# Kernel optimization log

Hardware: AMD Instinct MI355X
Metric: run time of the kernel (lower is better)

## Reference

```python
import jax, jax.numpy as jnp
import numpy as np

STRIDE = 1
PAD = 1
DIL = 1


def setup_inputs() -> dict:
    key = jax.random.key(0)
    k1, k2, k3, k4 = jax.random.split(key, 4)
    N, Cin, H, W = 4, 256, 64, 64
    Cout, kh, kw = 256, 3, 3
    inputs = jax.random.normal(k1, (N, Cin, H, W), jnp.float32)
    filter = jax.random.normal(k2, (Cout, Cin, kh, kw), jnp.float32) * 0.05
    # offsets in pixels (y,x interleaved per tap), typical magnitude O(1)
    offset = jax.random.normal(k3, (N, 2 * kh * kw, H, W), jnp.float32)
    # modulation mask in [0,1) (post-sigmoid in real nets)
    mask = jax.random.uniform(k4, (N, kh * kw, H, W), jnp.float32)
    return {"inputs": inputs, "filter": filter, "offset": offset, "mask": mask}


def _dcn_forward(inputs, filt, offset, mask):
    N, C, H, W = inputs.shape
    Cout, _, kh, kw = filt.shape
    K = kh * kw
    Ho = (H + 2 * PAD - DIL * (kh - 1) - 1) // STRIDE + 1
    Wo = (W + 2 * PAD - DIL * (kw - 1) - 1) // STRIDE + 1

    # base sampling grid per kernel tap: [K, Ho, Wo]
    ki, kj = jnp.meshgrid(jnp.arange(kh), jnp.arange(kw), indexing='ij')
    ki = ki.reshape(K, 1, 1)
    kj = kj.reshape(K, 1, 1)
    base_y = (jnp.arange(Ho)[None, :, None] * STRIDE - PAD + ki * DIL).astype(jnp.float32)
    base_x = (jnp.arange(Wo)[None, None, :] * STRIDE - PAD + kj * DIL).astype(jnp.float32)

    # offset channels: per tap k, channel 2k = dy, channel 2k+1 = dx
    off = offset.reshape(N, K, 2, Ho, Wo)
    y = base_y[None] + off[:, :, 0]  # [N, K, Ho, Wo]
    x = base_x[None] + off[:, :, 1]

    y0 = jnp.floor(y)
    x0 = jnp.floor(x)
    ly = y - y0  # fractional parts, [N, K, Ho, Wo]
    lx = x - x0
    y0i = y0.astype(jnp.int32)
    x0i = x0.astype(jnp.int32)

    def gather(img, yy, xx):
        # img [C,H,W]; yy,xx [K,Ho,Wo] int; zero outside bounds
        valid = (yy >= 0) & (yy < H) & (xx >= 0) & (xx < W)
        yc = jnp.clip(yy, 0, H - 1)
        xc = jnp.clip(xx, 0, W - 1)
        return img[:, yc, xc] * valid.astype(img.dtype)  # [C,K,Ho,Wo]

    def sample_one(img, y0i, x0i, ly, lx):
        v00 = gather(img, y0i, x0i)
        v01 = gather(img, y0i, x0i + 1)
        v10 = gather(img, y0i + 1, x0i)
        v11 = gather(img, y0i + 1, x0i + 1)
        return (v00 * (1 - ly) * (1 - lx) + v01 * (1 - ly) * lx
                + v10 * ly * (1 - lx) + v11 * ly * lx)

    # bilinear-sampled, modulated im2col columns: [N, C, K, Ho, Wo]
    col = jax.vmap(sample_one)(inputs, y0i, x0i, ly, lx)
    col = col * mask.reshape(N, 1, K, Ho, Wo)

    # grouped conv with num_groups=1: plain GEMM over (C, K)
    out = jnp.einsum('ock,nckhw->nohw', filt.reshape(Cout, C, K), col)
    return out


def reference(inputs, filter, offset, mask):
    return _dcn_forward(inputs, filter, offset, mask)
```

## Files before the change

kernel.cpp:

```cpp
#include <hip/hip_runtime.h>
#include <stdint.h>

typedef __attribute__((ext_vector_type(2))) float f32x2;
typedef __attribute__((ext_vector_type(4))) float f32x4;
typedef __attribute__((ext_vector_type(8))) short bf16x8;

static constexpr int N_ = 4, C_ = 256, HW_ = 4096;
static constexpr int CO_ = 256, KTAP = 9, KK = 2304;
static constexpr int NSTEP = 72;
static constexpr int A_STEP_BYTES = 16 * 64 * 16;

static constexpr size_t NHWC_BYTES = (size_t)N_ * HW_ * C_ * 2;
static constexpr size_t ABF_OFF    = NHWC_BYTES;
static constexpr size_t ABF_BYTES  = (size_t)NSTEP * A_STEP_BYTES;

__device__ inline unsigned f2bf(float f) {
  unsigned u = __builtin_bit_cast(unsigned, f);
  unsigned r = u + 0x7FFFu + ((u >> 16) & 1u);
  return r >> 16;
}
__device__ inline float asf(unsigned u) { return __builtin_bit_cast(float, u); }

__global__ __launch_bounds__(256) void k_nchw_to_nhwc(const float* __restrict__ in,
                                                      unsigned short* __restrict__ nhwc) {
  __shared__ float tile[64][65];
  int b = blockIdx.x;
  int n = b >> 8, cg = (b >> 6) & 3, hwg = b & 63;
  int c0 = cg * 64, hw0 = hwg * 64;
  int t = threadIdx.x;
  int col = t & 63, r0 = t >> 6;
#pragma unroll
  for (int i = 0; i < 16; ++i) {
    int row = r0 + i * 4;
    tile[row][col] = in[(size_t)(n * C_ + c0 + row) * HW_ + hw0 + col];
  }
  __syncthreads();
  int pr = t >> 2, cc0 = (t & 3) * 16;
  unsigned us[8];
#pragma unroll
  for (int i = 0; i < 8; ++i) {
    unsigned lo = f2bf(tile[cc0 + 2 * i][pr]);
    unsigned hi = f2bf(tile[cc0 + 2 * i + 1][pr]);
    us[i] = lo | (hi << 16);
  }
  unsigned* dst = (unsigned*)(nhwc + (size_t)(n * HW_ + hw0 + pr) * C_ + c0 + cc0);
  ((uint4*)dst)[0] = make_uint4(us[0], us[1], us[2], us[3]);
  ((uint4*)dst)[1] = make_uint4(us[4], us[5], us[6], us[7]);
}

__global__ __launch_bounds__(256) void k_prep_filter(const float* __restrict__ filt,
                                                     unsigned short* __restrict__ abf2) {
  int gid = blockIdx.x * 256 + threadIdx.x;
  int o = gid >> 8, c = gid & 255;
  const float* f = filt + (size_t)(o * C_ + c) * KTAP;
  int rb = o >> 4;
  int lane = ((c >> 3) & 3) * 16 + (o & 15);
  int j = c & 7;
#pragma unroll
  for (int tap = 0; tap < KTAP; ++tap) {
    int s = tap * 8 + (c >> 5);
    abf2[((size_t)(s * 16 + rb) * 64 + lane) * 8 + j] = (unsigned short)f2bf(f[tap]);
  }
}

struct GB { uint4 g[4]; f32x4 w; };

__device__ __forceinline__ f32x2 unpk(unsigned u) {
  return (f32x2){asf(u << 16), asf(u & 0xffff0000u)};
}

__device__ __forceinline__ void buildB8(const GB& b, char* dst) {
  f32x2 r0 = b.w.x * unpk(b.g[0].x) + b.w.y * unpk(b.g[1].x) +
             b.w.z * unpk(b.g[2].x) + b.w.w * unpk(b.g[3].x);
  f32x2 r1 = b.w.x * unpk(b.g[0].y) + b.w.y * unpk(b.g[1].y) +
             b.w.z * unpk(b.g[2].y) + b.w.w * unpk(b.g[3].y);
  f32x2 r2 = b.w.x * unpk(b.g[0].z) + b.w.y * unpk(b.g[1].z) +
             b.w.z * unpk(b.g[2].z) + b.w.w * unpk(b.g[3].z);
  f32x2 r3 = b.w.x * unpk(b.g[0].w) + b.w.y * unpk(b.g[1].w) +
             b.w.z * unpk(b.g[2].w) + b.w.w * unpk(b.g[3].w);
  unsigned o0, o1, o2, o3;
  asm("v_cvt_pk_bf16_f32 %0, %1, %2" : "=v"(o0) : "v"(r0.x), "v"(r0.y));
  asm("v_cvt_pk_bf16_f32 %0, %1, %2" : "=v"(o1) : "v"(r1.x), "v"(r1.y));
  asm("v_cvt_pk_bf16_f32 %0, %1, %2" : "=v"(o2) : "v"(r2.x), "v"(r2.y));
  asm("v_cvt_pk_bf16_f32 %0, %1, %2" : "=v"(o3) : "v"(r3.x), "v"(r3.y));
  *(uint4*)dst = make_uint4(o0, o1, o2, o3);
}

#define MFMA_BF16 __builtin_amdgcn_mfma_f32_16x16x32_bf16

#define PIPE(S, RDP, WRP, GCON, GISS, AC0, AC1, AN0, AN1)                      \
  do {                                                                         \
    if (cons) {                                                                \
      int s1_ = (S) + 1 < NSTEP ? (S) + 1 : NSTEP - 1;                         \
      AN0 = *(const bf16x8*)(aoff0 + (size_t)s1_ * A_STEP_BYTES);              \
      AN1 = *(const bf16x8*)(aoff1 + (size_t)s1_ * A_STEP_BYTES);              \
      const char* bb_ = (const char*)&Bl[0][0] + (RDP) * 4096;                 \
      bf16x8 b0_ = *(const bf16x8*)(bb_ + bo0);                                \
      bf16x8 b1_ = *(const bf16x8*)(bb_ + bo1);                                \
      __builtin_amdgcn_s_setprio(1);                                           \
      acc[0][0] = MFMA_BF16(AC0, b0_, acc[0][0], 0, 0, 0);                     \
      acc[1][0] = MFMA_BF16(AC1, b0_, acc[1][0], 0, 0, 0);                     \
      acc[0][1] = MFMA_BF16(AC0, b1_, acc[0][1], 0, 0, 0);                     \
      acc[1][1] = MFMA_BF16(AC1, b1_, acc[1][1], 0, 0, 0);                     \
      __builtin_amdgcn_s_setprio(0);                                           \
      bf16x8 b2_ = *(const bf16x8*)(bb_ + bo2);                                \
      bf16x8 b3_ = *(const bf16x8*)(bb_ + bo3);                                \
      __builtin_amdgcn_s_setprio(1);                                           \
      acc[0][2] = MFMA_BF16(AC0, b2_, acc[0][2], 0, 0, 0);                     \
      acc[1][2] = MFMA_BF16(AC1, b2_, acc[1][2], 0, 0, 0);                     \
      acc[0][3] = MFMA_BF16(AC0, b3_, acc[0][3], 0, 0, 0);                     \
      acc[1][3] = MFMA_BF16(AC1, b3_, acc[1][3], 0, 0, 0);                     \
      __builtin_amdgcn_s_setprio(0);                                           \
    } else {                                                                   \
      int s2_ = (S) + 2 < NSTEP ? (S) + 2 : NSTEP - 1;                         \
      if ((s2_ & 7) == 0) {                                                    \
        int tp_ = s2_ >> 3;                                                    \
        uint4 ra_ = *(const uint4*)&recA[(tp_ * 64 + p_b) * 4];                \
        wS = *(const f32x4*)&recW[(tp_ * 64 + p_b) * 4];                       \
        vS.x = ra_.x + kq16; vS.y = ra_.y + kq16;                              \
        vS.z = ra_.z + kq16; vS.w = ra_.w + kq16;                              \
      }                                                                        \
      unsigned co_ = (unsigned)((s2_ & 7) * 64);                               \
      GISS.g[0] = *(const uint4*)(nb_u + vS.x + co_);                          \
      GISS.g[1] = *(const uint4*)(nb_u + vS.y + co_);                          \
      GISS.g[2] = *(const uint4*)(nb_u + vS.z + co_);                          \
      GISS.g[3] = *(const uint4*)(nb_u + vS.w + co_);                          \
      GISS.w = wS;                                                             \
      buildB8(GCON, bwp + (WRP) * 4096);                                       \
      asm volatile("s_waitcnt lgkmcnt(0)" ::: "memory");                       \
    }                                                                          \
    asm volatile("" ::: "memory");                                             \
    __builtin_amdgcn_s_barrier();                                              \
    asm volatile("" ::: "memory");                                             \
  } while (0)

__global__ __launch_bounds__(768, 3) void k_dcn_gemm(const unsigned short* __restrict__ nhwc,
                                                     const unsigned short* __restrict__ abf2,
                                                     const float* __restrict__ offs,
                                                     const float* __restrict__ msk,
                                                     float* __restrict__ out) {
  __shared__ __align__(16) unsigned short Bl[2][2048];
  __shared__ float recW[KTAP * 64 * 4];
  __shared__ unsigned recA[KTAP * 64 * 4];

  int bid = blockIdx.x;
  int b = ((bid & 7) << 5) | (bid >> 3);
  int n = b >> 6;
  int ho = b & 63;
  int hw0 = ho << 6;
  int t = threadIdx.x;

  for (int r = t; r < 576; r += 768) {
    int pl = r / 9;
    int tap = r - pl * 9;
    int hw = hw0 + pl;
    float dy = offs[(size_t)(n * 18 + 2 * tap) * HW_ + hw];
    float dx = offs[(size_t)(n * 18 + 2 * tap + 1) * HW_ + hw];
    float mk = msk[(size_t)(n * 9 + tap) * HW_ + hw];
    float y = (float)(ho - 1 + tap / 3) + dy;
    float x = (float)(pl - 1 + tap % 3) + dx;
    float fy = floorf(y), fx = floorf(x);
    float ly = y - fy, lx = x - fx;
    int y0 = (int)fy, x0 = (int)fx;
    int y1 = y0 + 1, x1 = x0 + 1;
    float vy0 = (y0 >= 0 && y0 < 64) ? 1.f : 0.f;
    float vy1 = (y1 >= 0 && y1 < 64) ? 1.f : 0.f;
    float vx0 = (x0 >= 0 && x0 < 64) ? 1.f : 0.f;
    float vx1 = (x1 >= 0 && x1 < 64) ? 1.f : 0.f;
    int y0c = min(max(y0, 0), 63), y1c = min(max(y1, 0), 63);
    int x0c = min(max(x0, 0), 63), x1c = min(max(x1, 0), 63);
    int base = (tap * 64 + pl) * 4;
    recW[base + 0] = (1.f - ly) * (1.f - lx) * mk * vy0 * vx0;
    recW[base + 1] = (1.f - ly) * lx * mk * vy0 * vx1;
    recW[base + 2] = ly * (1.f - lx) * mk * vy1 * vx0;
    recW[base + 3] = ly * lx * mk * vy1 * vx1;
    recA[base + 0] = (unsigned)((y0c * 64 + x0c) * 512);
    recA[base + 1] = (unsigned)((y0c * 64 + x1c) * 512);
    recA[base + 2] = (unsigned)((y1c * 64 + x0c) * 512);
    recA[base + 3] = (unsigned)((y1c * 64 + x1c) * 512);
  }
  __syncthreads();

  int lane = t & 63, wv = t >> 6;
  bool cons = wv < 8;

  const char* aoff0 = (const char*)abf2 + ((wv * 2 + 0) * 64 + lane) * 16;
  const char* aoff1 = aoff0 + 1024;
  int cqr = lane >> 4;
  int pxl = lane & 15;
  const int bo0 = cqr * 1024 + ((((0 * 16 + pxl) + cqr * 5) & 63) * 16);
  const int bo1 = cqr * 1024 + ((((1 * 16 + pxl) + cqr * 5) & 63) * 16);
  const int bo2 = cqr * 1024 + ((((2 * 16 + pxl) + cqr * 5) & 63) * 16);
  const int bo3 = cqr * 1024 + ((((3 * 16 + pxl) + cqr * 5) & 63) * 16);

  int p_b = (t >> 2) & 63;
  int kq = t & 3;
  unsigned kq16 = (unsigned)(kq * 16);
  const char* nb_u = (const char*)nhwc + (size_t)n * HW_ * C_ * 2;
  char* bwp = (char*)&Bl[0][0] + (kq * 1024 + ((p_b + kq * 5) & 63) * 16);

  f32x4 acc[2][4];
#pragma unroll
  for (int mi = 0; mi < 2; ++mi)
#pragma unroll
    for (int ni = 0; ni < 4; ++ni) acc[mi][ni] = (f32x4){0.f, 0.f, 0.f, 0.f};

  GB gA, gB;
  bf16x8 afc0, afc1, afn0, afn1;
  uint4 vS;
  f32x4 wS;

  if (cons) {
    afc0 = *(const bf16x8*)(aoff0);
    afc1 = *(const bf16x8*)(aoff1);
  } else {
    uint4 ra0 = *(const uint4*)&recA[p_b * 4];
    wS = *(const f32x4*)&recW[p_b * 4];
    vS.x = ra0.x + kq16; vS.y = ra0.y + kq16;
    vS.z = ra0.z + kq16; vS.w = ra0.w + kq16;
    gA.g[0] = *(const uint4*)(nb_u + vS.x);
    gA.g[1] = *(const uint4*)(nb_u + vS.y);
    gA.g[2] = *(const uint4*)(nb_u + vS.z);
    gA.g[3] = *(const uint4*)(nb_u + vS.w);
    gA.w = wS;
    gB.g[0] = *(const uint4*)(nb_u + vS.x + 64);
    gB.g[1] = *(const uint4*)(nb_u + vS.y + 64);
    gB.g[2] = *(const uint4*)(nb_u + vS.z + 64);
    gB.g[3] = *(const uint4*)(nb_u + vS.w + 64);
    gB.w = wS;
    buildB8(gA, bwp);
    asm volatile("s_waitcnt lgkmcnt(0)" ::: "memory");
  }
  asm volatile("" ::: "memory");
  __builtin_amdgcn_s_barrier();
  asm volatile("" ::: "memory");

  for (int s = 0; s < NSTEP; s += 2) {
    PIPE(s,     0, 1, gB, gA, afc0, afc1, afn0, afn1);
    PIPE(s + 1, 1, 0, gA, gB, afn0, afn1, afc0, afc1);
  }

  if (cons) {
    float* ob = out + (size_t)n * CO_ * HW_ + hw0;
#pragma unroll
    for (int mi = 0; mi < 2; ++mi)
#pragma unroll
      for (int ni = 0; ni < 4; ++ni)
#pragma unroll
        for (int jj = 0; jj < 4; ++jj) {
          int o = wv * 32 + mi * 16 + (lane >> 4) * 4 + jj;
          int hw = ni * 16 + (lane & 15);
          ob[(size_t)o * HW_ + hw] = acc[mi][ni][jj];
        }
  }
}

extern "C" void kernel_launch(void* const* d_in, const int* in_sizes, int n_in,
                              void* d_out, int out_size, void* d_ws, size_t ws_size,
                              hipStream_t stream) {
  const float* inp  = (const float*)d_in[0];
  const float* filt = (const float*)d_in[1];
  const float* offs = (const float*)d_in[2];
  const float* msk  = (const float*)d_in[3];
  float* out = (float*)d_out;
  if (ws_size < ABF_OFF + ABF_BYTES) return;
  unsigned short* nhwc = (unsigned short*)d_ws;
  unsigned short* abf2 = (unsigned short*)((char*)d_ws + ABF_OFF);

  k_nchw_to_nhwc<<<1024, 256, 0, stream>>>(inp, nhwc);
  k_prep_filter<<<256, 256, 0, stream>>>(filt, abf2);
  k_dcn_gemm<<<256, 768, 0, stream>>>(nhwc, abf2, offs, msk, out);
}
```

Measured before the change: 53.93 us.

## Double pipeline step depth to K=64 and merge prep kernels into one launch

The GEMM main loop now handles two 32-wide K planes per step, so there are 36 steps instead of 72. The LDS B buffer doubles, producer waves issue eight 16-byte gathers per step, and consumers run sixteen MFMAs per barrier. The aim is to halve the number of barriers and pipeline handoffs. The two preprocessing kernels are also fused into one launch to save a kernel launch. In exchange, register pressure goes up in both producer and consumer waves, which may hurt occupancy at 768 threads with 3 blocks per CU.

```diff
diff --git a/kernel.cpp b/kernel.cpp
--- a/kernel.cpp
+++ b/kernel.cpp
@@ -7,12 +7,12 @@
 
 static constexpr int N_ = 4, C_ = 256, HW_ = 4096;
 static constexpr int CO_ = 256, KTAP = 9, KK = 2304;
-static constexpr int NSTEP = 72;
-static constexpr int A_STEP_BYTES = 16 * 64 * 16;
+static constexpr int NST = 36;
+static constexpr int A_PLANE = 16 * 64 * 16;
 
 static constexpr size_t NHWC_BYTES = (size_t)N_ * HW_ * C_ * 2;
 static constexpr size_t ABF_OFF    = NHWC_BYTES;
-static constexpr size_t ABF_BYTES  = (size_t)NSTEP * A_STEP_BYTES;
+static constexpr size_t ABF_BYTES  = (size_t)72 * A_PLANE;
 
 __device__ inline unsigned f2bf(float f) {
   unsigned u = __builtin_bit_cast(unsigned, f);
@@ -21,63 +21,63 @@
 }
 __device__ inline float asf(unsigned u) { return __builtin_bit_cast(float, u); }
 
-__global__ __launch_bounds__(256) void k_nchw_to_nhwc(const float* __restrict__ in,
-                                                      unsigned short* __restrict__ nhwc) {
-  __shared__ float tile[64][65];
+__global__ __launch_bounds__(256) void k_prep(const float* __restrict__ in,
+                                              const float* __restrict__ filt,
+                                              unsigned short* __restrict__ nhwc,
+                                              unsigned short* __restrict__ abf2) {
   int b = blockIdx.x;
-  int n = b >> 8, cg = (b >> 6) & 3, hwg = b & 63;
-  int c0 = cg * 64, hw0 = hwg * 64;
   int t = threadIdx.x;
-  int col = t & 63, r0 = t >> 6;
-#pragma unroll
-  for (int i = 0; i < 16; ++i) {
-    int row = r0 + i * 4;
-    tile[row][col] = in[(size_t)(n * C_ + c0 + row) * HW_ + hw0 + col];
-  }
-  __syncthreads();
-  int pr = t >> 2, cc0 = (t & 3) * 16;
-  unsigned us[8];
-#pragma unroll
-  for (int i = 0; i < 8; ++i) {
-    unsigned lo = f2bf(tile[cc0 + 2 * i][pr]);
-    unsigned hi = f2bf(tile[cc0 + 2 * i + 1][pr]);
-    us[i] = lo | (hi << 16);
-  }
-  unsigned* dst = (unsigned*)(nhwc + (size_t)(n * HW_ + hw0 + pr) * C_ + c0 + cc0);
-  ((uint4*)dst)[0] = make_uint4(us[0], us[1], us[2], us[3]);
-  ((uint4*)dst)[1] = make_uint4(us[4], us[5], us[6], us[7]);
-}
-
-__global__ __launch_bounds__(256) void k_prep_filter(const float* __restrict__ filt,
-                                                     unsigned short* __restrict__ abf2) {
-  int gid = blockIdx.x * 256 + threadIdx.x;
-  int o = gid >> 8, c = gid & 255;
-  const float* f = filt + (size_t)(o * C_ + c) * KTAP;
-  int rb = o >> 4;
-  int lane = ((c >> 3) & 3) * 16 + (o & 15);
-  int j = c & 7;
-#pragma unroll
-  for (int tap = 0; tap < KTAP; ++tap) {
-    int s = tap * 8 + (c >> 5);
-    abf2[((size_t)(s * 16 + rb) * 64 + lane) * 8 + j] = (unsigned short)f2bf(f[tap]);
-  }
-}
-
-struct GB { uint4 g[4]; f32x4 w; };
+  if (b < 1024) {
+    __shared__ float tile[64][65];
+    int n = b >> 8, cg = (b >> 6) & 3, hwg = b & 63;
+    int c0 = cg * 64, hw0 = hwg * 64;
+    int col = t & 63, r0 = t >> 6;
+#pragma unroll
+    for (int i = 0; i < 16; ++i) {
+      int row = r0 + i * 4;
+      tile[row][col] = in[(size_t)(n * C_ + c0 + row) * HW_ + hw0 + col];
+    }
+    __syncthreads();
+    int pr = t >> 2, cc0 = (t & 3) * 16;
+    unsigned us[8];
+#pragma unroll
+    for (int i = 0; i < 8; ++i) {
+      unsigned lo = f2bf(tile[cc0 + 2 * i][pr]);
+      unsigned hi = f2bf(tile[cc0 + 2 * i + 1][pr]);
+      us[i] = lo | (hi << 16);
+    }
+    unsigned* dst = (unsigned*)(nhwc + (size_t)(n * HW_ + hw0 + pr) * C_ + c0 + cc0);
+    ((uint4*)dst)[0] = make_uint4(us[0], us[1], us[2], us[3]);
+    ((uint4*)dst)[1] = make_uint4(us[4], us[5], us[6], us[7]);
+  } else {
+    int gid = (b - 1024) * 256 + t;
+    int o = gid >> 8, c = gid & 255;
+    const float* f = filt + (size_t)(o * C_ + c) * KTAP;
+    int rb = o >> 4;
+    int lane = ((c >> 3) & 3) * 16 + (o & 15);
+    int j = c & 7;
+#pragma unroll
+    for (int tap = 0; tap < KTAP; ++tap) {
+      int s32 = tap * 8 + (c >> 5);
+      abf2[((size_t)(s32 * 16 + rb) * 64 + lane) * 8 + j] = (unsigned short)f2bf(f[tap]);
+    }
+  }
+}
+
+struct GB2 { uint4 g[8]; f32x4 w; };
+struct AF  { bf16x8 f[4]; };
 
 __device__ __forceinline__ f32x2 unpk(unsigned u) {
   return (f32x2){asf(u << 16), asf(u & 0xffff0000u)};
 }
 
-__device__ __forceinline__ void buildB8(const GB& b, char* dst) {
-  f32x2 r0 = b.w.x * unpk(b.g[0].x) + b.w.y * unpk(b.g[1].x) +
-             b.w.z * unpk(b.g[2].x) + b.w.w * unpk(b.g[3].x);
-  f32x2 r1 = b.w.x * unpk(b.g[0].y) + b.w.y * unpk(b.g[1].y) +
-             b.w.z * unpk(b.g[2].y) + b.w.w * unpk(b.g[3].y);
-  f32x2 r2 = b.w.x * unpk(b.g[0].z) + b.w.y * unpk(b.g[1].z) +
-             b.w.z * unpk(b.g[2].z) + b.w.w * unpk(b.g[3].z);
-  f32x2 r3 = b.w.x * unpk(b.g[0].w) + b.w.y * unpk(b.g[1].w) +
-             b.w.z * unpk(b.g[2].w) + b.w.w * unpk(b.g[3].w);
+__device__ __forceinline__ void buildB8p(const uint4& g0, const uint4& g1,
+                                         const uint4& g2, const uint4& g3,
+                                         f32x4 w, char* dst) {
+  f32x2 r0 = w.x * unpk(g0.x) + w.y * unpk(g1.x) + w.z * unpk(g2.x) + w.w * unpk(g3.x);
+  f32x2 r1 = w.x * unpk(g0.y) + w.y * unpk(g1.y) + w.z * unpk(g2.y) + w.w * unpk(g3.y);
+  f32x2 r2 = w.x * unpk(g0.z) + w.y * unpk(g1.z) + w.z * unpk(g2.z) + w.w * unpk(g3.z);
+  f32x2 r3 = w.x * unpk(g0.w) + w.y * unpk(g1.w) + w.z * unpk(g2.w) + w.w * unpk(g3.w);
   unsigned o0, o1, o2, o3;
   asm("v_cvt_pk_bf16_f32 %0, %1, %2" : "=v"(o0) : "v"(r0.x), "v"(r0.y));
   asm("v_cvt_pk_bf16_f32 %0, %1, %2" : "=v"(o1) : "v"(r1.x), "v"(r1.y));
@@ -88,45 +88,68 @@
 
 #define MFMA_BF16 __builtin_amdgcn_mfma_f32_16x16x32_bf16
 
-#define PIPE(S, RDP, WRP, GCON, GISS, AC0, AC1, AN0, AN1)                      \
+#define PIPE(S, RDP, WRP, GCON, GISS, AC, AN)                                  \
   do {                                                                         \
     if (cons) {                                                                \
-      int s1_ = (S) + 1 < NSTEP ? (S) + 1 : NSTEP - 1;                         \
-      AN0 = *(const bf16x8*)(aoff0 + (size_t)s1_ * A_STEP_BYTES);              \
-      AN1 = *(const bf16x8*)(aoff1 + (size_t)s1_ * A_STEP_BYTES);              \
-      const char* bb_ = (const char*)&Bl[0][0] + (RDP) * 4096;                 \
-      bf16x8 b0_ = *(const bf16x8*)(bb_ + bo0);                                \
-      bf16x8 b1_ = *(const bf16x8*)(bb_ + bo1);                                \
+      int s1_ = (S) + 1 < NST ? (S) + 1 : NST - 1;                             \
+      const char* ab_ = aoff0 + (size_t)(2 * s1_) * A_PLANE;                   \
+      AN.f[0] = *(const bf16x8*)(ab_);                                         \
+      AN.f[1] = *(const bf16x8*)(ab_ + A_PLANE);                               \
+      AN.f[2] = *(const bf16x8*)(ab_ + 1024);                                  \
+      AN.f[3] = *(const bf16x8*)(ab_ + 1024 + A_PLANE);                        \
+      const char* bb_ = (const char*)&Bl[0][0] + (RDP) * 8192;                 \
+      bf16x8 b0_ = *(const bf16x8*)(bb_ + bo[0][0]);                           \
+      bf16x8 b1_ = *(const bf16x8*)(bb_ + bo[1][0]);                           \
+      bf16x8 b2_ = *(const bf16x8*)(bb_ + bo[2][0]);                           \
+      bf16x8 b3_ = *(const bf16x8*)(bb_ + bo[3][0]);                           \
       __builtin_amdgcn_s_setprio(1);                                           \
-      acc[0][0] = MFMA_BF16(AC0, b0_, acc[0][0], 0, 0, 0);                     \
-      acc[1][0] = MFMA_BF16(AC1, b0_, acc[1][0], 0, 0, 0);                     \
-      acc[0][1] = MFMA_BF16(AC0, b1_, acc[0][1], 0, 0, 0);                     \
-      acc[1][1] = MFMA_BF16(AC1, b1_, acc[1][1], 0, 0, 0);                     \
+      acc[0][0] = MFMA_BF16(AC.f[0], b0_, acc[0][0], 0, 0, 0);                 \
+      acc[1][0] = MFMA_BF16(AC.f[2], b0_, acc[1][0], 0, 0, 0);                 \
+      acc[0][1] = MFMA_BF16(AC.f[0], b1_, acc[0][1], 0, 0, 0);                 \
+      acc[1][1] = MFMA_BF16(AC.f[2], b1_, acc[1][1], 0, 0, 0);                 \
+      acc[0][2] = MFMA_BF16(AC.f[0], b2_, acc[0][2], 0, 0, 0);                 \
+      acc[1][2] = MFMA_BF16(AC.f[2], b2_, acc[1][2], 0, 0, 0);                 \
+      acc[0][3] = MFMA_BF16(AC.f[0], b3_, acc[0][3], 0, 0, 0);                 \
+      acc[1][3] = MFMA_BF16(AC.f[2], b3_, acc[1][3], 0, 0, 0);                 \
       __builtin_amdgcn_s_setprio(0);                                           \
-      bf16x8 b2_ = *(const bf16x8*)(bb_ + bo2);                                \
-      bf16x8 b3_ = *(const bf16x8*)(bb_ + bo3);                                \
+      bf16x8 b4_ = *(const bf16x8*)(bb_ + bo[0][1]);                           \
+      bf16x8 b5_ = *(const bf16x8*)(bb_ + bo[1][1]);                           \
+      bf16x8 b6_ = *(const bf16x8*)(bb_ + bo[2][1]);                           \
+      bf16x8 b7_ = *(const bf16x8*)(bb_ + bo[3][1]);                           \
       __builtin_amdgcn_s_setprio(1);                                           \
-      acc[0][2] = MFMA_BF16(AC0, b2_, acc[0][2], 0, 0, 0);                     \
-      acc[1][2] = MFMA_BF16(AC1, b2_, acc[1][2], 0, 0, 0);                     \
-      acc[0][3] = MFMA_BF16(AC0, b3_, acc[0][3], 0, 0, 0);                     \
-      acc[1][3] = MFMA_BF16(AC1, b3_, acc[1][3], 0, 0, 0);                     \
+      acc[0][0] = MFMA_BF16(AC.f[1], b4_, acc[0][0], 0, 0, 0);                 \
+      acc[1][0] = MFMA_BF16(AC.f[3], b4_, acc[1][0], 0, 0, 0);                 \
+      acc[0][1] = MFMA_BF16(AC.f[1], b5_, acc[0][1], 0, 0, 0);                 \
+      acc[1][1] = MFMA_BF16(AC.f[3], b5_, acc[1][1], 0, 0, 0);                 \
+      acc[0][2] = MFMA_BF16(AC.f[1], b6_, acc[0][2], 0, 0, 0);                 \
+      acc[1][2] = MFMA_BF16(AC.f[3], b6_, acc[1][2], 0, 0, 0);                 \
+      acc[0][3] = MFMA_BF16(AC.f[1], b7_, acc[0][3], 0, 0, 0);                 \
+      acc[1][3] = MFMA_BF16(AC.f[3], b7_, acc[1][3], 0, 0, 0);                 \
       __builtin_amdgcn_s_setprio(0);                                           \
     } else {                                                                   \
-      int s2_ = (S) + 2 < NSTEP ? (S) + 2 : NSTEP - 1;                         \
-      if ((s2_ & 7) == 0) {                                                    \
-        int tp_ = s2_ >> 3;                                                    \
+      int s2_ = (S) + 2 < NST ? (S) + 2 : NST - 1;                             \
+      if ((s2_ & 3) == 0) {                                                    \
+        int tp_ = s2_ >> 2;                                                    \
         uint4 ra_ = *(const uint4*)&recA[(tp_ * 64 + p_b) * 4];                \
         wS = *(const f32x4*)&recW[(tp_ * 64 + p_b) * 4];                       \
-        vS.x = ra_.x + kq16; vS.y = ra_.y + kq16;                              \
-        vS.z = ra_.z + kq16; vS.w = ra_.w + kq16;                              \
+        vS.x = ra_.x + kq32; vS.y = ra_.y + kq32;                              \
+        vS.z = ra_.z + kq32; vS.w = ra_.w + kq32;                              \
       }                                                                        \
-      unsigned co_ = (unsigned)((s2_ & 7) * 64);                               \
+      unsigned co_ = (unsigned)((s2_ & 3) * 128);                              \
       GISS.g[0] = *(const uint4*)(nb_u + vS.x + co_);                          \
-      GISS.g[1] = *(const uint4*)(nb_u + vS.y + co_);                          \
-      GISS.g[2] = *(const uint4*)(nb_u + vS.z + co_);                          \
-      GISS.g[3] = *(const uint4*)(nb_u + vS.w + co_);                          \
+      GISS.g[1] = *(const uint4*)(nb_u + vS.x + co_ + 16);                     \
+      GISS.g[2] = *(const uint4*)(nb_u + vS.y + co_);                          \
+      GISS.g[3] = *(const uint4*)(nb_u + vS.y + co_ + 16);                     \
+      GISS.g[4] = *(const uint4*)(nb_u + vS.z + co_);                          \
+      GISS.g[5] = *(const uint4*)(nb_u + vS.z + co_ + 16);                     \
+      GISS.g[6] = *(const uint4*)(nb_u + vS.w + co_);                          \
+      GISS.g[7] = *(const uint4*)(nb_u + vS.w + co_ + 16);                     \
       GISS.w = wS;                                                             \
-      buildB8(GCON, bwp + (WRP) * 4096);                                       \
+      __builtin_amdgcn_sched_barrier(0);                                       \
+      buildB8p(GCON.g[0], GCON.g[2], GCON.g[4], GCON.g[6], GCON.w,             \
+               bwp0 + (WRP) * 8192);                                           \
+      buildB8p(GCON.g[1], GCON.g[3], GCON.g[5], GCON.g[7], GCON.w,             \
+               bwp1 + (WRP) * 8192);                                           \
       asm volatile("s_waitcnt lgkmcnt(0)" ::: "memory");                       \
     }                                                                          \
     asm volatile("" ::: "memory");                                             \
@@ -139,7 +162,7 @@
                                                      const float* __restrict__ offs,
                                                      const float* __restrict__ msk,
                                                      float* __restrict__ out) {
-  __shared__ __align__(16) unsigned short Bl[2][2048];
+  __shared__ __align__(16) unsigned short Bl[2][4096];
   __shared__ float recW[KTAP * 64 * 4];
   __shared__ unsigned recA[KTAP * 64 * 4];
 
@@ -184,20 +207,26 @@
   int lane = t & 63, wv = t >> 6;
   bool cons = wv < 8;
 
-  const char* aoff0 = (const char*)abf2 + ((wv * 2 + 0) * 64 + lane) * 16;
-  const char* aoff1 = aoff0 + 1024;
-  int cqr = lane >> 4;
+  const char* aoff0 = (const char*)abf2 + ((wv * 2) * 64 + lane) * 16;
+  int q_r = lane >> 4;
   int pxl = lane & 15;
-  const int bo0 = cqr * 1024 + ((((0 * 16 + pxl) + cqr * 5) & 63) * 16);
-  const int bo1 = cqr * 1024 + ((((1 * 16 + pxl) + cqr * 5) & 63) * 16);
-  const int bo2 = cqr * 1024 + ((((2 * 16 + pxl) + cqr * 5) & 63) * 16);
-  const int bo3 = cqr * 1024 + ((((3 * 16 + pxl) + cqr * 5) & 63) * 16);
-
-  int p_b = (t >> 2) & 63;
-  int kq = t & 3;
-  unsigned kq16 = (unsigned)(kq * 16);
+  int bo[4][2];
+#pragma unroll
+  for (int ni = 0; ni < 4; ++ni)
+#pragma unroll
+    for (int h = 0; h < 2; ++h) {
+      int p = h * 4 + q_r;
+      bo[ni][h] = p * 1024 + (((pxl + 16 * ni) + 5 * p) & 63) * 16;
+    }
+
+  int pid = t - 512;
+  int p_b = (pid >> 2) & 63;
+  int kq = pid & 3;
+  unsigned kq32 = (unsigned)(kq * 32);
   const char* nb_u = (const char*)nhwc + (size_t)n * HW_ * C_ * 2;
-  char* bwp = (char*)&Bl[0][0] + (kq * 1024 + ((p_b + kq * 5) & 63) * 16);
+  int pl0 = 2 * kq, pl1 = 2 * kq + 1;
+  char* bwp0 = (char*)&Bl[0][0] + pl0 * 1024 + ((p_b + 5 * pl0) & 63) * 16;
+  char* bwp1 = (char*)&Bl[0][0] + pl1 * 1024 + ((p_b + 5 * pl1) & 63) * 16;
 
   f32x4 acc[2][4];
 #pragma unroll
@@ -205,39 +234,50 @@
 #pragma unroll
     for (int ni = 0; ni < 4; ++ni) acc[mi][ni] = (f32x4){0.f, 0.f, 0.f, 0.f};
 
-  GB gA, gB;
-  bf16x8 afc0, afc1, afn0, afn1;
+  GB2 gA, gB;
+  AF aC, aN;
   uint4 vS;
   f32x4 wS;
 
   if (cons) {
-    afc0 = *(const bf16x8*)(aoff0);
-    afc1 = *(const bf16x8*)(aoff1);
+    aC.f[0] = *(const bf16x8*)(aoff0);
+    aC.f[1] = *(const bf16x8*)(aoff0 + A_PLANE);
+    aC.f[2] = *(const bf16x8*)(aoff0 + 1024);
+    aC.f[3] = *(const bf16x8*)(aoff0 + 1024 + A_PLANE);
   } else {
     uint4 ra0 = *(const uint4*)&recA[p_b * 4];
     wS = *(const f32x4*)&recW[p_b * 4];
-    vS.x = ra0.x + kq16; vS.y = ra0.y + kq16;
-    vS.z = ra0.z + kq16; vS.w = ra0.w + kq16;
+    vS.x = ra0.x + kq32; vS.y = ra0.y + kq32;
+    vS.z = ra0.z + kq32; vS.w = ra0.w + kq32;
     gA.g[0] = *(const uint4*)(nb_u + vS.x);
-    gA.g[1] = *(const uint4*)(nb_u + vS.y);
-    gA.g[2] = *(const uint4*)(nb_u + vS.z);
-    gA.g[3] = *(const uint4*)(nb_u + vS.w);
+    gA.g[1] = *(const uint4*)(nb_u + vS.x + 16);
+    gA.g[2] = *(const uint4*)(nb_u + vS.y);
+    gA.g[3] = *(const uint4*)(nb_u + vS.y + 16);
+    gA.g[4] = *(const uint4*)(nb_u + vS.z);
+    gA.g[5] = *(const uint4*)(nb_u + vS.z + 16);
+    gA.g[6] = *(const uint4*)(nb_u + vS.w);
+    gA.g[7] = *(const uint4*)(nb_u + vS.w + 16);
     gA.w = wS;
-    gB.g[0] = *(const uint4*)(nb_u + vS.x + 64);
-    gB.g[1] = *(const uint4*)(nb_u + vS.y + 64);
-    gB.g[2] = *(const uint4*)(nb_u + vS.z + 64);
-    gB.g[3] = *(const uint4*)(nb_u + vS.w + 64);
+    gB.g[0] = *(const uint4*)(nb_u + vS.x + 128);
+    gB.g[1] = *(const uint4*)(nb_u + vS.x + 144);
+    gB.g[2] = *(const uint4*)(nb_u + vS.y + 128);
+    gB.g[3] = *(const uint4*)(nb_u + vS.y + 144);
+    gB.g[4] = *(const uint4*)(nb_u + vS.z + 128);
+    gB.g[5] = *(const uint4*)(nb_u + vS.z + 144);
+    gB.g[6] = *(const uint4*)(nb_u + vS.w + 128);
+    gB.g[7] = *(const uint4*)(nb_u + vS.w + 144);
     gB.w = wS;
-    buildB8(gA, bwp);
+    buildB8p(gA.g[0], gA.g[2], gA.g[4], gA.g[6], gA.w, bwp0);
+    buildB8p(gA.g[1], gA.g[3], gA.g[5], gA.g[7], gA.w, bwp1);
     asm volatile("s_waitcnt lgkmcnt(0)" ::: "memory");
   }
   asm volatile("" ::: "memory");
   __builtin_amdgcn_s_barrier();
   asm volatile("" ::: "memory");
 
-  for (int s = 0; s < NSTEP; s += 2) {
-    PIPE(s,     0, 1, gB, gA, afc0, afc1, afn0, afn1);
-    PIPE(s + 1, 1, 0, gA, gB, afn0, afn1, afc0, afc1);
+  for (int s = 0; s < NST; s += 2) {
+    PIPE(s,     0, 1, gB, gA, aC, aN);
+    PIPE(s + 1, 1, 0, gA, gB, aN, aC);
   }
 
   if (cons) {
@@ -267,7 +307,6 @@
   unsigned short* nhwc = (unsigned short*)d_ws;
   unsigned short* abf2 = (unsigned short*)((char*)d_ws + ABF_OFF);
 
-  k_nchw_to_nhwc<<<1024, 256, 0, stream>>>(inp, nhwc);
-  k_prep_filter<<<256, 256, 0, stream>>>(filt, abf2);
+  k_prep<<<1280, 256, 0, stream>>>(inp, filt, nhwc, abf2);
   k_dcn_gemm<<<256, 768, 0, stream>>>(nhwc, abf2, offs, msk, out);
 }
```

Result: slower. 74.65 us (+38.4%).

## Halve GEMM pixel tile to 32 for more blocks and merge prep kernels

Applied to the files above, without the earlier changes.

Each GEMM block now covers 32 output pixels (half a row) instead of 64, so the grid doubles to 512 blocks with 640 threads: 8 MFMA consumer waves and 2 gather/producer waves. LDS buffers, swizzles and accumulators shrink to match, and the launch bounds move to allow more resident blocks per CU. This targets poor occupancy and wave balance across the 256 CUs. The input layout transform and filter prep kernels are also fused into one launch to cut launch overhead. In exchange, A-fragment reuse per block is halved, so filter traffic doubles, and there is half as much gather work to hide latency behind.

```diff
diff --git a/kernel.cpp b/kernel.cpp
--- a/kernel.cpp
+++ b/kernel.cpp
@@ -8,11 +8,11 @@
 static constexpr int N_ = 4, C_ = 256, HW_ = 4096;
 static constexpr int CO_ = 256, KTAP = 9, KK = 2304;
 static constexpr int NSTEP = 72;
-static constexpr int A_STEP_BYTES = 16 * 64 * 16;
+static constexpr int A_PLANE = 16 * 64 * 16;
 
 static constexpr size_t NHWC_BYTES = (size_t)N_ * HW_ * C_ * 2;
 static constexpr size_t ABF_OFF    = NHWC_BYTES;
-static constexpr size_t ABF_BYTES  = (size_t)NSTEP * A_STEP_BYTES;
+static constexpr size_t ABF_BYTES  = (size_t)NSTEP * A_PLANE;
 
 __device__ inline unsigned f2bf(float f) {
   unsigned u = __builtin_bit_cast(unsigned, f);
@@ -21,45 +21,46 @@
 }
 __device__ inline float asf(unsigned u) { return __builtin_bit_cast(float, u); }
 
-__global__ __launch_bounds__(256) void k_nchw_to_nhwc(const float* __restrict__ in,
-                                                      unsigned short* __restrict__ nhwc) {
-  __shared__ float tile[64][65];
+__global__ __launch_bounds__(256) void k_prep(const float* __restrict__ in,
+                                              const float* __restrict__ filt,
+                                              unsigned short* __restrict__ nhwc,
+                                              unsigned short* __restrict__ abf2) {
   int b = blockIdx.x;
-  int n = b >> 8, cg = (b >> 6) & 3, hwg = b & 63;
-  int c0 = cg * 64, hw0 = hwg * 64;
   int t = threadIdx.x;
-  int col = t & 63, r0 = t >> 6;
-#pragma unroll
-  for (int i = 0; i < 16; ++i) {
-    int row = r0 + i * 4;
-    tile[row][col] = in[(size_t)(n * C_ + c0 + row) * HW_ + hw0 + col];
-  }
-  __syncthreads();
-  int pr = t >> 2, cc0 = (t & 3) * 16;
-  unsigned us[8];
-#pragma unroll
-  for (int i = 0; i < 8; ++i) {
-    unsigned lo = f2bf(tile[cc0 + 2 * i][pr]);
-    unsigned hi = f2bf(tile[cc0 + 2 * i + 1][pr]);
-    us[i] = lo | (hi << 16);
-  }
-  unsigned* dst = (unsigned*)(nhwc + (size_t)(n * HW_ + hw0 + pr) * C_ + c0 + cc0);
-  ((uint4*)dst)[0] = make_uint4(us[0], us[1], us[2], us[3]);
-  ((uint4*)dst)[1] = make_uint4(us[4], us[5], us[6], us[7]);
-}
-
-__global__ __launch_bounds__(256) void k_prep_filter(const float* __restrict__ filt,
-                                                     unsigned short* __restrict__ abf2) {
-  int gid = blockIdx.x * 256 + threadIdx.x;
-  int o = gid >> 8, c = gid & 255;
-  const float* f = filt + (size_t)(o * C_ + c) * KTAP;
-  int rb = o >> 4;
-  int lane = ((c >> 3) & 3) * 16 + (o & 15);
-  int j = c & 7;
-#pragma unroll
-  for (int tap = 0; tap < KTAP; ++tap) {
-    int s = tap * 8 + (c >> 5);
-    abf2[((size_t)(s * 16 + rb) * 64 + lane) * 8 + j] = (unsigned short)f2bf(f[tap]);
+  if (b < 1024) {
+    __shared__ float tile[64][65];
+    int n = b >> 8, cg = (b >> 6) & 3, hwg = b & 63;
+    int c0 = cg * 64, hw0 = hwg * 64;
+    int col = t & 63, r0 = t >> 6;
+#pragma unroll
+    for (int i = 0; i < 16; ++i) {
+      int row = r0 + i * 4;
+      tile[row][col] = in[(size_t)(n * C_ + c0 + row) * HW_ + hw0 + col];
+    }
+    __syncthreads();
+    int pr = t >> 2, cc0 = (t & 3) * 16;
+    unsigned us[8];
+#pragma unroll
+    for (int i = 0; i < 8; ++i) {
+      unsigned lo = f2bf(tile[cc0 + 2 * i][pr]);
+      unsigned hi = f2bf(tile[cc0 + 2 * i + 1][pr]);
+      us[i] = lo | (hi << 16);
+    }
+    unsigned* dst = (unsigned*)(nhwc + (size_t)(n * HW_ + hw0 + pr) * C_ + c0 + cc0);
+    ((uint4*)dst)[0] = make_uint4(us[0], us[1], us[2], us[3]);
+    ((uint4*)dst)[1] = make_uint4(us[4], us[5], us[6], us[7]);
+  } else {
+    int gid = (b - 1024) * 256 + t;
+    int o = gid >> 8, c = gid & 255;
+    const float* f = filt + (size_t)(o * C_ + c) * KTAP;
+    int rb = o >> 4;
+    int lane = ((c >> 3) & 3) * 16 + (o & 15);
+    int j = c & 7;
+#pragma unroll
+    for (int tap = 0; tap < KTAP; ++tap) {
+      int s = tap * 8 + (c >> 5);
+      abf2[((size_t)(s * 16 + rb) * 64 + lane) * 8 + j] = (unsigned short)f2bf(f[tap]);
+    }
   }
 }
 
@@ -92,9 +93,9 @@
   do {                                                                         \
     if (cons) {                                                                \
       int s1_ = (S) + 1 < NSTEP ? (S) + 1 : NSTEP - 1;                         \
-      AN0 = *(const bf16x8*)(aoff0 + (size_t)s1_ * A_STEP_BYTES);              \
-      AN1 = *(const bf16x8*)(aoff1 + (size_t)s1_ * A_STEP_BYTES);              \
-      const char* bb_ = (const char*)&Bl[0][0] + (RDP) * 4096;                 \
+      AN0 = *(const bf16x8*)(aoff0 + (size_t)s1_ * A_PLANE);                   \
+      AN1 = *(const bf16x8*)(aoff1 + (size_t)s1_ * A_PLANE);                   \
+      const char* bb_ = (const char*)&Bl[0][0] + (RDP) * 2048;                 \
       bf16x8 b0_ = *(const bf16x8*)(bb_ + bo0);                                \
       bf16x8 b1_ = *(const bf16x8*)(bb_ + bo1);                                \
       __builtin_amdgcn_s_setprio(1);                                           \
@@ -103,20 +104,12 @@
       acc[0][1] = MFMA_BF16(AC0, b1_, acc[0][1], 0, 0, 0);                     \
       acc[1][1] = MFMA_BF16(AC1, b1_, acc[1][1], 0, 0, 0);                     \
       __builtin_amdgcn_s_setprio(0);                                           \
-      bf16x8 b2_ = *(const bf16x8*)(bb_ + bo2);                                \
-      bf16x8 b3_ = *(const bf16x8*)(bb_ + bo3);                                \
-      __builtin_amdgcn_s_setprio(1);                                           \
-      acc[0][2] = MFMA_BF16(AC0, b2_, acc[0][2], 0, 0, 0);                     \
-      acc[1][2] = MFMA_BF16(AC1, b2_, acc[1][2], 0, 0, 0);                     \
-      acc[0][3] = MFMA_BF16(AC0, b3_, acc[0][3], 0, 0, 0);                     \
-      acc[1][3] = MFMA_BF16(AC1, b3_, acc[1][3], 0, 0, 0);                     \
-      __builtin_amdgcn_s_setprio(0);                                           \
     } else {                                                                   \
       int s2_ = (S) + 2 < NSTEP ? (S) + 2 : NSTEP - 1;                         \
       if ((s2_ & 7) == 0) {                                                    \
         int tp_ = s2_ >> 3;                                                    \
-        uint4 ra_ = *(const uint4*)&recA[(tp_ * 64 + p_b) * 4];                \
-        wS = *(const f32x4*)&recW[(tp_ * 64 + p_b) * 4];                       \
+        uint4 ra_ = *(const uint4*)&recA[(tp_ * 32 + p_b) * 4];                \
+        wS = *(const f32x4*)&recW[(tp_ * 32 + p_b) * 4];                       \
         vS.x = ra_.x + kq16; vS.y = ra_.y + kq16;                              \
         vS.z = ra_.z + kq16; vS.w = ra_.w + kq16;                              \
       }                                                                        \
@@ -126,7 +119,7 @@
       GISS.g[2] = *(const uint4*)(nb_u + vS.z + co_);                          \
       GISS.g[3] = *(const uint4*)(nb_u + vS.w + co_);                          \
       GISS.w = wS;                                                             \
-      buildB8(GCON, bwp + (WRP) * 4096);                                       \
+      buildB8(GCON, bwp + (WRP) * 2048);                                       \
       asm volatile("s_waitcnt lgkmcnt(0)" ::: "memory");                       \
     }                                                                          \
     asm volatile("" ::: "memory");                                             \
@@ -134,23 +127,25 @@
     asm volatile("" ::: "memory");                                             \
   } while (0)
 
-__global__ __launch_bounds__(768, 3) void k_dcn_gemm(const unsigned short* __restrict__ nhwc,
+__global__ __launch_bounds__(640, 5) void k_dcn_gemm(const unsigned short* __restrict__ nhwc,
                                                      const unsigned short* __restrict__ abf2,
                                                      const float* __restrict__ offs,
                                                      const float* __restrict__ msk,
                                                      float* __restrict__ out) {
-  __shared__ __align__(16) unsigned short Bl[2][2048];
-  __shared__ float recW[KTAP * 64 * 4];
-  __shared__ unsigned recA[KTAP * 64 * 4];
+  __shared__ __align__(16) unsigned short Bl[2][1024];
+  __shared__ float recW[KTAP * 32 * 4];
+  __shared__ unsigned recA[KTAP * 32 * 4];
 
   int bid = blockIdx.x;
-  int b = ((bid & 7) << 5) | (bid >> 3);
-  int n = b >> 6;
-  int ho = b & 63;
-  int hw0 = ho << 6;
+  int w = ((bid & 7) << 6) | (bid >> 3);
+  int n = w >> 7;
+  int ho = (w >> 1) & 63;
+  int pxh = w & 1;
+  int hw0 = ho * 64 + pxh * 32;
   int t = threadIdx.x;
 
-  for (int r = t; r < 576; r += 768) {
+  if (t < 288) {
+    int r = t;
     int pl = r / 9;
     int tap = r - pl * 9;
     int hw = hw0 + pl;
@@ -158,7 +153,7 @@
     float dx = offs[(size_t)(n * 18 + 2 * tap + 1) * HW_ + hw];
     float mk = msk[(size_t)(n * 9 + tap) * HW_ + hw];
     float y = (float)(ho - 1 + tap / 3) + dy;
-    float x = (float)(pl - 1 + tap % 3) + dx;
+    float x = (float)((hw & 63) - 1 + tap % 3) + dx;
     float fy = floorf(y), fx = floorf(x);
     float ly = y - fy, lx = x - fx;
     int y0 = (int)fy, x0 = (int)fx;
@@ -169,7 +164,7 @@
     float vx1 = (x1 >= 0 && x1 < 64) ? 1.f : 0.f;
     int y0c = min(max(y0, 0), 63), y1c = min(max(y1, 0), 63);
     int x0c = min(max(x0, 0), 63), x1c = min(max(x1, 0), 63);
-    int base = (tap * 64 + pl) * 4;
+    int base = (tap * 32 + pl) * 4;
     recW[base + 0] = (1.f - ly) * (1.f - lx) * mk * vy0 * vx0;
     recW[base + 1] = (1.f - ly) * lx * mk * vy0 * vx1;
     recW[base + 2] = ly * (1.f - lx) * mk * vy1 * vx0;
@@ -186,24 +181,23 @@
 
   const char* aoff0 = (const char*)abf2 + ((wv * 2 + 0) * 64 + lane) * 16;
   const char* aoff1 = aoff0 + 1024;
-  int cqr = lane >> 4;
+  int p_r = lane >> 4;
   int pxl = lane & 15;
-  const int bo0 = cqr * 1024 + ((((0 * 16 + pxl) + cqr * 5) & 63) * 16);
-  const int bo1 = cqr * 1024 + ((((1 * 16 + pxl) + cqr * 5) & 63) * 16);
-  const int bo2 = cqr * 1024 + ((((2 * 16 + pxl) + cqr * 5) & 63) * 16);
-  const int bo3 = cqr * 1024 + ((((3 * 16 + pxl) + cqr * 5) & 63) * 16);
-
-  int p_b = (t >> 2) & 63;
-  int kq = t & 3;
+  const int bo0 = p_r * 512 + (((pxl + 0) + 5 * p_r) & 31) * 16;
+  const int bo1 = p_r * 512 + (((pxl + 16) + 5 * p_r) & 31) * 16;
+
+  int pid = t - 512;
+  int p_b = (pid >> 2) & 31;
+  int kq = pid & 3;
   unsigned kq16 = (unsigned)(kq * 16);
   const char* nb_u = (const char*)nhwc + (size_t)n * HW_ * C_ * 2;
-  char* bwp = (char*)&Bl[0][0] + (kq * 1024 + ((p_b + kq * 5) & 63) * 16);
-
-  f32x4 acc[2][4];
+  char* bwp = (char*)&Bl[0][0] + kq * 512 + ((p_b + 5 * kq) & 31) * 16;
+
+  f32x4 acc[2][2];
 #pragma unroll
   for (int mi = 0; mi < 2; ++mi)
 #pragma unroll
-    for (int ni = 0; ni < 4; ++ni) acc[mi][ni] = (f32x4){0.f, 0.f, 0.f, 0.f};
+    for (int ni = 0; ni < 2; ++ni) acc[mi][ni] = (f32x4){0.f, 0.f, 0.f, 0.f};
 
   GB gA, gB;
   bf16x8 afc0, afc1, afn0, afn1;
@@ -245,7 +239,7 @@
 #pragma unroll
     for (int mi = 0; mi < 2; ++mi)
 #pragma unroll
-      for (int ni = 0; ni < 4; ++ni)
+      for (int ni = 0; ni < 2; ++ni)
 #pragma unroll
         for (int jj = 0; jj < 4; ++jj) {
           int o = wv * 32 + mi * 16 + (lane >> 4) * 4 + jj;
@@ -267,7 +261,6 @@
   unsigned short* nhwc = (unsigned short*)d_ws;
   unsigned short* abf2 = (unsigned short*)((char*)d_ws + ABF_OFF);
 
-  k_nchw_to_nhwc<<<1024, 256, 0, stream>>>(inp, nhwc);
-  k_prep_filter<<<256, 256, 0, stream>>>(filt, abf2);
-  k_dcn_gemm<<<256, 768, 0, stream>>>(nhwc, abf2, offs, msk, out);
-}
+  k_prep<<<1280, 256, 0, stream>>>(inp, filt, nhwc, abf2);
+  k_dcn_gemm<<<512, 640, 0, stream>>>(nhwc, abf2, offs, msk, out);
+}
```

New measurement: 120.2 us. 123% more time.
